# Optimization experiments

Measured on AMD Instinct MI355X. Metric: run time of the kernel, lower is better.

## Reference

```python
import jax, jax.numpy as jnp
import numpy as np

D_MODEL, N_HEADS, LATENT, ROPE = 4096, 128, 512, 64
HEAD_DIM = D_MODEL // N_HEADS  # 32
B, S = 2, 1024


def setup_inputs() -> dict:
    key = jax.random.key(0)
    ks = jax.random.split(key, 9)
    def w(k, i, o):
        return jax.random.normal(k, (i, o), dtype=jnp.float32) * (1.0 / np.sqrt(i))
    return {
        "x": jax.random.normal(ks[0], (B, S, D_MODEL), dtype=jnp.float32),
        "Wq_down": w(ks[1], D_MODEL, LATENT),
        "Wq_up": w(ks[2], LATENT, N_HEADS * HEAD_DIM),
        "Wq_rope": w(ks[3], D_MODEL, N_HEADS * ROPE),
        "Wkv_down": w(ks[4], D_MODEL, LATENT),
        "Wk_up": w(ks[5], LATENT, N_HEADS * HEAD_DIM),
        "Wv_up": w(ks[6], LATENT, N_HEADS * HEAD_DIM),
        "Wk_rope": w(ks[7], D_MODEL, ROPE),
        "Wo": w(ks[8], N_HEADS * HEAD_DIM, D_MODEL),
    }


def reference(x, Wq_down, Wq_up, Wq_rope, Wkv_down, Wk_up, Wv_up, Wk_rope, Wo):
    b, s, _ = x.shape
    # latent down-projections
    c_q = x @ Wq_down                                   # [B,S,latent]
    c_kv = x @ Wkv_down                                 # [B,S,latent]
    # up-projections, reshaped to per-head
    q_c = (c_q @ Wq_up).reshape(b, s, N_HEADS, HEAD_DIM)    # [B,S,H,Dh]
    q_r = (x @ Wq_rope).reshape(b, s, N_HEADS, ROPE)        # [B,S,H,Dr]
    k_c = (c_kv @ Wk_up).reshape(b, s, N_HEADS, HEAD_DIM)   # [B,S,H,Dh]
    v_c = (c_kv @ Wv_up).reshape(b, s, N_HEADS, HEAD_DIM)   # [B,S,H,Dh]
    k_r = x @ Wk_rope                                       # [B,S,Dr] shared over heads
    scale = jnp.asarray((HEAD_DIM + ROPE) ** 0.5, x.dtype)
    # scores = q.k with q=[q_c|q_r], k=[k_c|k_r(broadcast)] -> split the dot product
    scores = (jnp.einsum("bqhd,bkhd->bhqk", q_c, k_c)
              + jnp.einsum("bqhd,bkd->bhqk", q_r, k_r)) / scale  # [B,H,S,S]
    attn = jax.nn.softmax(scores, axis=-1)
    out = jnp.einsum("bhqk,bkhd->bqhd", attn, v_c)          # [B,S,H,Dh]
    out = out.reshape(b, s, N_HEADS * HEAD_DIM)
    return out @ Wo                                         # [B,S,d_model]
```

## Files before the change

kernel.cpp:

```cpp
#include <hip/hip_runtime.h>
#include <hip/hip_bf16.h>
#include <math.h>

#define D_MODEL 4096
#define N_HEADS 128
#define LATENT  512
#define ROPE_D  64
#define HEAD_D  32
#define BATCH   2
#define SEQ     1024
#define NTOK    (BATCH*SEQ)

typedef unsigned short u16;
typedef __attribute__((ext_vector_type(8))) short bf16x8;
typedef __attribute__((ext_vector_type(4))) float f32x4;

__device__ __forceinline__ u16 f2bf(float f) {
    union { float f; unsigned u; } v; v.f = f;
    unsigned r = (v.u + 0x7fffu + ((v.u >> 16) & 1u)) >> 16;
    return (u16)r;
}

__device__ __forceinline__ void gl_lds16(const u16* g, u16* l) {
    __builtin_amdgcn_global_load_lds(
        (const __attribute__((address_space(1))) unsigned int*)g,
        (__attribute__((address_space(3))) unsigned int*)l, 16, 0, 0);
}

__global__ __launch_bounds__(256)
void cast_x_kernel(const float* __restrict__ in, u16* __restrict__ out)
{
    size_t i = ((size_t)blockIdx.x * 256 + threadIdx.x) * 8;
    float4 a = *(const float4*)(in + i);
    float4 b = *(const float4*)(in + i + 4);
    u16 o[8] = {f2bf(a.x), f2bf(a.y), f2bf(a.z), f2bf(a.w),
                f2bf(b.x), f2bf(b.y), f2bf(b.z), f2bf(b.w)};
    *(bf16x8*)(out + i) = *(bf16x8*)o;
}

__global__ __launch_bounds__(256)
void castT_kernel(const float* __restrict__ W, u16* __restrict__ Wt,
                  int K, int N)
{
    __shared__ float tile[32][33];
    const int tid = threadIdx.x;
    const int j0 = blockIdx.x * 32;
    const int i0 = blockIdx.y * 32;
    #pragma unroll
    for (int it = 0; it < 4; ++it) {
        int e = tid + it * 256;
        int r = e >> 5, c = e & 31;
        tile[r][c] = (j0 + c < N) ? W[(size_t)(i0 + r) * N + j0 + c] : 0.f;
    }
    __syncthreads();
    #pragma unroll
    for (int it = 0; it < 4; ++it) {
        int e = tid + it * 256;
        int n = e >> 5, k = e & 31;
        Wt[(size_t)(j0 + n) * K + i0 + k] = f2bf(tile[k][n]);
    }
}

template<int BN_, int OUTF32>
__global__ __launch_bounds__(512)
void gemm256(const u16* __restrict__ A, const u16* __restrict__ Bt,
             void* __restrict__ Cout, int M, int N, int K,
             int lda, int ldb, int ldc)
{
    constexpr int WN   = BN_ / 4;
    constexpr int NFR  = WN / 16;
    constexpr int BUFE = 8192 + BN_ * 32;

    extern __shared__ __align__(16) u16 lds[];

    const int tid  = threadIdx.x;
    const int lane = tid & 63;
    const int wave = tid >> 6;
    const int wr = wave >> 2, wc = wave & 3;
    const int l15 = lane & 15, lg = lane >> 4;

    const int nwg  = gridDim.x * gridDim.y;
    const int orig = blockIdx.y * gridDim.x + blockIdx.x;
    const int swz  = (orig & 7) * (nwg >> 3) + (orig >> 3);
    const int bm = (swz / gridDim.x) * 256, bn = (swz % gridDim.x) * BN_;

    const int NT = K >> 5;

    auto stage = [&](int t) {
        const int buf = t & 3;
        u16* bA = lds + buf * BUFE;
        u16* bB = bA + 8192;
        const int kt = t * 32;
        #pragma unroll
        for (int it = 0; it < 2; ++it) {
            int f = it * 512 + tid;
            int row = f >> 2, c = f & 3;
            int sc = (c ^ (row >> 1)) & 3;
            gl_lds16(A + (size_t)(bm + row) * lda + kt + sc * 8, bA + f * 8);
        }
        #pragma unroll
        for (int it = 0; it < BN_ / 128; ++it) {
            int f = it * 512 + tid;
            int row = f >> 2, c = f & 3;
            int sc = (c ^ (row >> 1)) & 3;
            gl_lds16(Bt + (size_t)(bn + row) * ldb + kt + sc * 8, bB + f * 8);
        }
    };

    f32x4 acc[8][NFR];
    #pragma unroll
    for (int m = 0; m < 8; ++m)
        #pragma unroll
        for (int n = 0; n < NFR; ++n) acc[m][n] = (f32x4){0.f, 0.f, 0.f, 0.f};

    stage(0); stage(1); stage(2);

    for (int t = 0; t < NT; ++t) {
        const int rem = NT - 1 - t;
        if constexpr (BN_ == 256) {
            if (rem >= 2)      asm volatile("s_waitcnt vmcnt(8)" ::: "memory");
            else if (rem == 1) asm volatile("s_waitcnt vmcnt(4)" ::: "memory");
            else               asm volatile("s_waitcnt vmcnt(0)" ::: "memory");
        } else {
            if (rem >= 2)      asm volatile("s_waitcnt vmcnt(6)" ::: "memory");
            else if (rem == 1) asm volatile("s_waitcnt vmcnt(3)" ::: "memory");
            else               asm volatile("s_waitcnt vmcnt(0)" ::: "memory");
        }
        __builtin_amdgcn_s_barrier();
        asm volatile("" ::: "memory");

        if (t + 3 < NT) stage(t + 3);

        const u16* bA = lds + (t & 3) * BUFE;
        const u16* bB = bA + 8192;

        bf16x8 af[8], bfr[NFR];
        #pragma unroll
        for (int m = 0; m < 8; ++m) {
            int row = wr * 128 + m * 16 + l15;
            af[m] = *(const bf16x8*)(bA + row * 32 + (((lg ^ (row >> 1)) & 3) << 3));
        }
        #pragma unroll
        for (int n = 0; n < NFR; ++n) {
            int row = wc * WN + n * 16 + l15;
            bfr[n] = *(const bf16x8*)(bB + row * 32 + (((lg ^ (row >> 1)) & 3) << 3));
        }
        __builtin_amdgcn_s_setprio(1);
        #pragma unroll
        for (int m = 0; m < 8; ++m)
            #pragma unroll
            for (int n = 0; n < NFR; ++n)
                acc[m][n] = __builtin_amdgcn_mfma_f32_16x16x32_bf16(
                    af[m], bfr[n], acc[m][n], 0, 0, 0);
        __builtin_amdgcn_s_setprio(0);
    }

    #pragma unroll
    for (int m = 0; m < 8; ++m)
        #pragma unroll
        for (int n = 0; n < NFR; ++n)
            #pragma unroll
            for (int ri = 0; ri < 4; ++ri) {
                int row = bm + wr * 128 + m * 16 + 4 * lg + ri;
                int col = bn + wc * WN + n * 16 + l15;
                if (col < N) {
                    float v = acc[m][n][ri];
                    if (OUTF32) ((float*)Cout)[(size_t)row * ldc + col] = v;
                    else        ((u16*)Cout)[(size_t)row * ldc + col] = f2bf(v);
                }
            }
}

__global__ __launch_bounds__(256)
void vtrans_kernel(const u16* __restrict__ vc, u16* __restrict__ vt)
{
    __shared__ __align__(16) u16 tile[64][72];
    const int tid = threadIdx.x;
    const int c0 = blockIdx.x * 64;
    const int s0 = blockIdx.y * 64;
    const int b  = blockIdx.z;
    #pragma unroll
    for (int it = 0; it < 2; ++it) {
        int e = it * 256 + tid;
        int r = e >> 3, c8 = e & 7;
        *(bf16x8*)&tile[r][c8 * 8] =
            *(const bf16x8*)(vc + (size_t)(b * SEQ + s0 + r) * 8192 + c0 + c8 * 8);
    }
    __syncthreads();
    #pragma unroll
    for (int it = 0; it < 2; ++it) {
        int e = it * 256 + tid;
        int d = e >> 3, c8 = e & 7;
        u16 o[8];
        #pragma unroll
        for (int j = 0; j < 8; ++j) o[j] = tile[c8 * 8 + j][d];
        *(bf16x8*)(vt + (size_t)(b * D_MODEL + c0 + d) * SEQ + s0 + c8 * 8) = *(bf16x8*)o;
    }
}

__global__ __launch_bounds__(256)
void attn_kernel(const u16* __restrict__ q_c, const u16* __restrict__ q_r,
                 const u16* __restrict__ k_c, const u16* __restrict__ k_r,
                 const u16* __restrict__ vt,  u16* __restrict__ attn_out)
{
    __shared__ __align__(16) u16 s_kc[2][64 * 32];
    __shared__ __align__(16) u16 s_kr[2][64 * 64];
    __shared__ __align__(16) u16 s_vt[2][32 * 64];
    __shared__ __align__(16) u16 s_p[4][16 * 64];

    const int tid  = threadIdx.x;
    const int lane = tid & 63;
    const int w    = tid >> 6;
    const int l15  = lane & 15, lg = lane >> 4;
    const int q0 = blockIdx.x * 64;
    const int h  = blockIdx.y;
    const int b  = blockIdx.z;
    const size_t bS = (size_t)b * SEQ;
    const int hc = h * HEAD_D;
    const float c2 = 0.1020620726159658f * 1.44269504088896f;

    const int qrow = q0 + w * 16 + l15;
    const bf16x8 qf0 = *(const bf16x8*)(q_c + (bS + qrow) * 4096 + hc + lg * 8);
    const bf16x8 qf1 = *(const bf16x8*)(q_r + (bS + qrow) * 9344 + h * ROPE_D + lg * 8);
    const bf16x8 qf2 = *(const bf16x8*)(q_r + (bS + qrow) * 9344 + h * ROPE_D + 32 + lg * 8);

    float m2 = -1e30f, lsum = 0.f;
    f32x4 oacc[2];
    oacc[0] = (f32x4){0.f, 0.f, 0.f, 0.f};
    oacc[1] = (f32x4){0.f, 0.f, 0.f, 0.f};

    auto stage = [&](int buf, int k0) {
        { int f = tid, r = f >> 2, c = f & 3;
          gl_lds16(k_c + (bS + k0 + r) * 8192 + hc + ((c ^ (r & 3)) << 3),
                   &s_kc[buf][f * 8]); }
        #pragma unroll
        for (int it = 0; it < 2; ++it) {
          int f = it * 256 + tid, r = f >> 3, c = f & 7;
          gl_lds16(k_r + (bS + k0 + r) * 9344 + ((c ^ (r & 7)) << 3),
                   &s_kr[buf][f * 8]); }
        { int f = tid, d = f >> 3, c = f & 7;
          gl_lds16(vt + ((size_t)b * D_MODEL + hc + d) * SEQ + k0 + ((c ^ (d & 7)) << 3),
                   &s_vt[buf][f * 8]); }
    };

    stage(0, 0);
    __syncthreads();

    int cur = 0;
    for (int t = 0; t < SEQ / 64; ++t) {
        if (t + 1 < SEQ / 64) stage(cur ^ 1, (t + 1) * 64);

        f32x4 sc[4];
        #pragma unroll
        for (int fc = 0; fc < 4; ++fc) sc[fc] = (f32x4){0.f, 0.f, 0.f, 0.f};
        __builtin_amdgcn_s_setprio(1);
        #pragma unroll
        for (int fc = 0; fc < 4; ++fc) {
            int row = fc * 16 + l15;
            bf16x8 kb = *(const bf16x8*)&s_kc[cur][row * 32 + ((lg ^ (row & 3)) << 3)];
            sc[fc] = __builtin_amdgcn_mfma_f32_16x16x32_bf16(kb, qf0, sc[fc], 0, 0, 0);
        }
        #pragma unroll
        for (int tt = 0; tt < 2; ++tt) {
            bf16x8 qf = tt ? qf2 : qf1;
            #pragma unroll
            for (int fc = 0; fc < 4; ++fc) {
                int row = fc * 16 + l15;
                bf16x8 kb = *(const bf16x8*)&s_kr[cur][row * 64 + (((tt * 4 + lg) ^ (row & 7)) << 3)];
                sc[fc] = __builtin_amdgcn_mfma_f32_16x16x32_bf16(kb, qf, sc[fc], 0, 0, 0);
            }
        }
        __builtin_amdgcn_s_setprio(0);

        float tmx = sc[0][0];
        #pragma unroll
        for (int fc = 0; fc < 4; ++fc)
            #pragma unroll
            for (int ri = 0; ri < 4; ++ri)
                tmx = fmaxf(tmx, sc[fc][ri]);
        tmx = fmaxf(tmx, __shfl_xor(tmx, 16));
        tmx = fmaxf(tmx, __shfl_xor(tmx, 32));
        float tl2 = tmx * c2;
        if (!__all(tl2 <= m2 + 8.f)) {
            float mn = fmaxf(m2, tl2);
            float corr = exp2f(m2 - mn);
            m2 = mn;
            lsum *= corr;
            #pragma unroll
            for (int ri = 0; ri < 4; ++ri) {
                float cr = __shfl(corr, 4 * lg + ri);
                oacc[0][ri] *= cr; oacc[1][ri] *= cr;
            }
        }
        float rs = 0.f;
        unsigned pk0[4], pk1[4];
        #pragma unroll
        for (int fc = 0; fc < 4; ++fc) {
            float p0 = exp2f(fmaf(sc[fc][0], c2, -m2));
            float p1 = exp2f(fmaf(sc[fc][1], c2, -m2));
            float p2 = exp2f(fmaf(sc[fc][2], c2, -m2));
            float p3 = exp2f(fmaf(sc[fc][3], c2, -m2));
            rs += (p0 + p1) + (p2 + p3);
            asm("v_cvt_pk_bf16_f32 %0, %1, %2" : "=v"(pk0[fc]) : "v"(p0), "v"(p1));
            asm("v_cvt_pk_bf16_f32 %0, %1, %2" : "=v"(pk1[fc]) : "v"(p2), "v"(p3));
        }
        rs += __shfl_xor(rs, 16);
        rs += __shfl_xor(rs, 32);
        lsum += rs;
        #pragma unroll
        for (int fc = 0; fc < 4; ++fc) {
            int ch = (2 * fc + (lg >> 1)) ^ (l15 & 7);
            *(uint2*)&s_p[w][l15 * 64 + ch * 8 + 4 * (lg & 1)] =
                make_uint2(pk0[fc], pk1[fc]);
        }

        __builtin_amdgcn_s_setprio(1);
        #pragma unroll
        for (int t2 = 0; t2 < 2; ++t2) {
            bf16x8 pa = *(const bf16x8*)&s_p[w][l15 * 64 + (((t2 * 4 + lg) ^ (l15 & 7)) << 3)];
            #pragma unroll
            for (int fd = 0; fd < 2; ++fd) {
                int row = fd * 16 + l15;
                bf16x8 vb = *(const bf16x8*)&s_vt[cur][row * 64 + (((t2 * 4 + lg) ^ (row & 7)) << 3)];
                oacc[fd] = __builtin_amdgcn_mfma_f32_16x16x32_bf16(pa, vb, oacc[fd], 0, 0, 0);
            }
        }
        __builtin_amdgcn_s_setprio(0);

        __syncthreads();
        cur ^= 1;
    }

    #pragma unroll
    for (int ri = 0; ri < 4; ++ri) {
        float ls = __shfl(lsum, 4 * lg + ri);
        float inv = 1.f / ls;
        int row = q0 + w * 16 + 4 * lg + ri;
        attn_out[(bS + row) * 4096 + hc + l15]      = f2bf(oacc[0][ri] * inv);
        attn_out[(bS + row) * 4096 + hc + 16 + l15] = f2bf(oacc[1][ri] * inv);
    }
}

extern "C" void kernel_launch(void* const* d_in, const int* in_sizes, int n_in,
                              void* d_out, int out_size, void* d_ws, size_t ws_size,
                              hipStream_t stream)
{
    (void)in_sizes; (void)n_in; (void)out_size; (void)ws_size;

    const float* x        = (const float*)d_in[0];
    const float* Wq_down  = (const float*)d_in[1];
    const float* Wq_up    = (const float*)d_in[2];
    const float* Wq_rope  = (const float*)d_in[3];
    const float* Wkv_down = (const float*)d_in[4];
    const float* Wk_up    = (const float*)d_in[5];
    const float* Wv_up    = (const float*)d_in[6];
    const float* Wk_rope  = (const float*)d_in[7];
    const float* Wo       = (const float*)d_in[8];

    u16* ws   = (u16*)d_ws;
    u16* xb   = ws;
    u16* BigT = xb + (size_t)8388608;
    u16* UpT  = BigT + (size_t)38797312;
    u16* WuqT = UpT + (size_t)4194304;
    u16* C_big= WuqT + (size_t)2097152;
    u16* C2   = C_big + (size_t)19136512;
    u16* WoT  = BigT;
    u16* vt   = BigT + (size_t)16777216;
    u16* q_c  = BigT + (size_t)25165824;
    u16* attn_out = xb;

    dim3 blk(256);

    (void)hipFuncSetAttribute((const void*)&gemm256<256,0>,
                              hipFuncAttributeMaxDynamicSharedMemorySize, 131072);
    (void)hipFuncSetAttribute((const void*)&gemm256<128,0>,
                              hipFuncAttributeMaxDynamicSharedMemorySize, 98304);
    (void)hipFuncSetAttribute((const void*)&gemm256<128,1>,
                              hipFuncAttributeMaxDynamicSharedMemorySize, 98304);

    hipMemsetAsync(BigT + (size_t)9280 * 4096, 0, (size_t)192 * 4096 * 2, stream);
    hipLaunchKernelGGL(cast_x_kernel, dim3(4096), blk, 0, stream, x, xb);
    hipLaunchKernelGGL(castT_kernel, dim3(256, 128), blk, 0, stream, Wq_rope, BigT, 4096, 8192);
    hipLaunchKernelGGL(castT_kernel, dim3(16, 128), blk, 0, stream, Wq_down, BigT + (size_t)8192 * 4096, 4096, 512);
    hipLaunchKernelGGL(castT_kernel, dim3(16, 128), blk, 0, stream, Wkv_down, BigT + (size_t)8704 * 4096, 4096, 512);
    hipLaunchKernelGGL(castT_kernel, dim3(2, 128), blk, 0, stream, Wk_rope, BigT + (size_t)9216 * 4096, 4096, 64);
    hipLaunchKernelGGL(castT_kernel, dim3(128, 16), blk, 0, stream, Wk_up, UpT, 512, 4096);
    hipLaunchKernelGGL(castT_kernel, dim3(128, 16), blk, 0, stream, Wv_up, UpT + (size_t)4096 * 512, 512, 4096);
    hipLaunchKernelGGL(castT_kernel, dim3(128, 16), blk, 0, stream, Wq_up, WuqT, 512, 4096);

    gemm256<256,0><<<dim3(37, 8), dim3(512), 131072, stream>>>(
        xb, BigT, C_big, NTOK, 9344, 4096, 4096, 4096, 9344);
    hipLaunchKernelGGL(castT_kernel, dim3(128, 128), blk, 0, stream, Wo, WoT, 4096, 4096);
    gemm256<256,0><<<dim3(32, 8), dim3(512), 131072, stream>>>(
        C_big + 8704, UpT, C2, NTOK, 8192, 512, 9344, 512, 8192);
    gemm256<128,0><<<dim3(32, 8), dim3(512), 98304, stream>>>(
        C_big + 8192, WuqT, q_c, NTOK, 4096, 512, 9344, 512, 4096);
    hipLaunchKernelGGL(vtrans_kernel, dim3(64, 16, 2), blk, 0, stream, C2 + 4096, vt);
    hipLaunchKernelGGL(attn_kernel, dim3(16, 128, 2), blk, 0, stream,
                       q_c, C_big, C2, C_big + 9216, vt, attn_out);
    gemm256<128,1><<<dim3(32, 8), dim3(512), 98304, stream>>>(
        attn_out, WoT, d_out, NTOK, 4096, 4096, 4096, 4096, 4096);
}
```

Before: 604.9 us.

## Replace GEMM with 256x128 BK64 triple-buffered ping-pong pipeline

Replaces the templated 256xBN GEMM (BK=32, 4-stage) with a single 256x128 tile kernel using BK=64, three LDS slots, an 8-chunk XOR swizzle, and split A/B prefetch issued across two half-steps. Barriers with sched_barrier fences wrap each MFMA cluster, aiming for a ping-pong style schedule that overlaps loads with compute. All GEMMs now use BN=128 with larger grids. The column bound check is dropped and the zero padding memset is shrunk to match the narrower tile rounding (9344 is a multiple of 128). The cost is more barriers per K step and fewer MFMAs per LDS read for the former BN=256 calls.

```diff
diff --git a/kernel.cpp b/kernel.cpp
--- a/kernel.cpp
+++ b/kernel.cpp
@@ -61,15 +61,15 @@
     }
 }
 
-template<int BN_, int OUTF32>
+template<int OUTF32>
 __global__ __launch_bounds__(512)
-void gemm256(const u16* __restrict__ A, const u16* __restrict__ Bt,
-             void* __restrict__ Cout, int M, int N, int K,
-             int lda, int ldb, int ldc)
-{
-    constexpr int WN   = BN_ / 4;
-    constexpr int NFR  = WN / 16;
-    constexpr int BUFE = 8192 + BN_ * 32;
+void gemm8p(const u16* __restrict__ A, const u16* __restrict__ Bt,
+            void* __restrict__ Cout, int M, int N, int K,
+            int lda, int ldb, int ldc)
+{
+    constexpr int TILE_A = 256 * 64;
+    constexpr int TILE_B = 128 * 64;
+    constexpr int SLOT   = TILE_A + TILE_B;
 
     extern __shared__ __align__(16) u16 lds[];
 
@@ -82,92 +82,102 @@
     const int nwg  = gridDim.x * gridDim.y;
     const int orig = blockIdx.y * gridDim.x + blockIdx.x;
     const int swz  = (orig & 7) * (nwg >> 3) + (orig >> 3);
-    const int bm = (swz / gridDim.x) * 256, bn = (swz % gridDim.x) * BN_;
-
-    const int NT = K >> 5;
-
-    auto stage = [&](int t) {
-        const int buf = t & 3;
-        u16* bA = lds + buf * BUFE;
-        u16* bB = bA + 8192;
-        const int kt = t * 32;
+    const int bm = (swz / gridDim.x) * 256, bn = (swz % gridDim.x) * 128;
+
+    const int NT = K >> 6;
+
+    auto stageA = [&](int t) {
+        u16* base = lds + (t % 3) * SLOT;
+        const int kt = t << 6;
+        #pragma unroll
+        for (int it = 0; it < 4; ++it) {
+            int f = it * 512 + tid;
+            int row = f >> 3, c = f & 7;
+            int sc = c ^ (row & 7);
+            gl_lds16(A + (size_t)(bm + row) * lda + kt + sc * 8, base + f * 8);
+        }
+    };
+    auto stageB = [&](int t) {
+        u16* base = lds + (t % 3) * SLOT + TILE_A;
+        const int kt = t << 6;
         #pragma unroll
         for (int it = 0; it < 2; ++it) {
             int f = it * 512 + tid;
-            int row = f >> 2, c = f & 3;
-            int sc = (c ^ (row >> 1)) & 3;
-            gl_lds16(A + (size_t)(bm + row) * lda + kt + sc * 8, bA + f * 8);
-        }
-        #pragma unroll
-        for (int it = 0; it < BN_ / 128; ++it) {
-            int f = it * 512 + tid;
-            int row = f >> 2, c = f & 3;
-            int sc = (c ^ (row >> 1)) & 3;
-            gl_lds16(Bt + (size_t)(bn + row) * ldb + kt + sc * 8, bB + f * 8);
+            int row = f >> 3, c = f & 7;
+            int sc = c ^ (row & 7);
+            gl_lds16(Bt + (size_t)(bn + row) * ldb + kt + sc * 8, base + f * 8);
         }
     };
 
-    f32x4 acc[8][NFR];
+    f32x4 acc[8][2];
+    #pragma unroll
+    for (int m = 0; m < 8; ++m) {
+        acc[m][0] = (f32x4){0.f, 0.f, 0.f, 0.f};
+        acc[m][1] = (f32x4){0.f, 0.f, 0.f, 0.f};
+    }
+
+    stageA(0); stageB(0); stageA(1); stageB(1);
+    asm volatile("s_waitcnt vmcnt(6)" ::: "memory");
+    __builtin_amdgcn_sched_barrier(0);
+    __builtin_amdgcn_s_barrier();
+    __builtin_amdgcn_sched_barrier(0);
+
+    for (int t = 0; t < NT; ++t) {
+        const u16* bA = lds + (t % 3) * SLOT;
+        const u16* bB = bA + TILE_A;
+        #pragma unroll
+        for (int s = 0; s < 2; ++s) {
+            bf16x8 af[8], bfr[2];
+            #pragma unroll
+            for (int m = 0; m < 8; ++m) {
+                int row = wr * 128 + m * 16 + l15;
+                int ch = (s * 4 + lg) ^ (row & 7);
+                af[m] = *(const bf16x8*)(bA + row * 64 + ch * 8);
+            }
+            #pragma unroll
+            for (int n = 0; n < 2; ++n) {
+                int row = wc * 32 + n * 16 + l15;
+                int ch = (s * 4 + lg) ^ (row & 7);
+                bfr[n] = *(const bf16x8*)(bB + row * 64 + ch * 8);
+            }
+            if (s == 0) {
+                if (t + 2 < NT) stageA(t + 2);
+            } else {
+                if (t + 2 < NT) stageB(t + 2);
+                if (t + 1 < NT) {
+                    if (t + 2 < NT) asm volatile("s_waitcnt vmcnt(6)" ::: "memory");
+                    else            asm volatile("s_waitcnt vmcnt(0)" ::: "memory");
+                }
+            }
+            asm volatile("" ::: "memory");
+            __builtin_amdgcn_sched_barrier(0);
+            __builtin_amdgcn_s_barrier();
+            __builtin_amdgcn_sched_barrier(0);
+            __builtin_amdgcn_s_setprio(1);
+            #pragma unroll
+            for (int m = 0; m < 8; ++m) {
+                acc[m][0] = __builtin_amdgcn_mfma_f32_16x16x32_bf16(af[m], bfr[0], acc[m][0], 0, 0, 0);
+                acc[m][1] = __builtin_amdgcn_mfma_f32_16x16x32_bf16(af[m], bfr[1], acc[m][1], 0, 0, 0);
+            }
+            __builtin_amdgcn_s_setprio(0);
+            __builtin_amdgcn_sched_barrier(0);
+            __builtin_amdgcn_s_barrier();
+            __builtin_amdgcn_sched_barrier(0);
+            asm volatile("" ::: "memory");
+        }
+    }
+
     #pragma unroll
     for (int m = 0; m < 8; ++m)
         #pragma unroll
-        for (int n = 0; n < NFR; ++n) acc[m][n] = (f32x4){0.f, 0.f, 0.f, 0.f};
-
-    stage(0); stage(1); stage(2);
-
-    for (int t = 0; t < NT; ++t) {
-        const int rem = NT - 1 - t;
-        if constexpr (BN_ == 256) {
-            if (rem >= 2)      asm volatile("s_waitcnt vmcnt(8)" ::: "memory");
-            else if (rem == 1) asm volatile("s_waitcnt vmcnt(4)" ::: "memory");
-            else               asm volatile("s_waitcnt vmcnt(0)" ::: "memory");
-        } else {
-            if (rem >= 2)      asm volatile("s_waitcnt vmcnt(6)" ::: "memory");
-            else if (rem == 1) asm volatile("s_waitcnt vmcnt(3)" ::: "memory");
-            else               asm volatile("s_waitcnt vmcnt(0)" ::: "memory");
-        }
-        __builtin_amdgcn_s_barrier();
-        asm volatile("" ::: "memory");
-
-        if (t + 3 < NT) stage(t + 3);
-
-        const u16* bA = lds + (t & 3) * BUFE;
-        const u16* bB = bA + 8192;
-
-        bf16x8 af[8], bfr[NFR];
-        #pragma unroll
-        for (int m = 0; m < 8; ++m) {
-            int row = wr * 128 + m * 16 + l15;
-            af[m] = *(const bf16x8*)(bA + row * 32 + (((lg ^ (row >> 1)) & 3) << 3));
-        }
-        #pragma unroll
-        for (int n = 0; n < NFR; ++n) {
-            int row = wc * WN + n * 16 + l15;
-            bfr[n] = *(const bf16x8*)(bB + row * 32 + (((lg ^ (row >> 1)) & 3) << 3));
-        }
-        __builtin_amdgcn_s_setprio(1);
-        #pragma unroll
-        for (int m = 0; m < 8; ++m)
-            #pragma unroll
-            for (int n = 0; n < NFR; ++n)
-                acc[m][n] = __builtin_amdgcn_mfma_f32_16x16x32_bf16(
-                    af[m], bfr[n], acc[m][n], 0, 0, 0);
-        __builtin_amdgcn_s_setprio(0);
-    }
-
-    #pragma unroll
-    for (int m = 0; m < 8; ++m)
-        #pragma unroll
-        for (int n = 0; n < NFR; ++n)
+        for (int n = 0; n < 2; ++n)
             #pragma unroll
             for (int ri = 0; ri < 4; ++ri) {
                 int row = bm + wr * 128 + m * 16 + 4 * lg + ri;
-                int col = bn + wc * WN + n * 16 + l15;
-                if (col < N) {
-                    float v = acc[m][n][ri];
-                    if (OUTF32) ((float*)Cout)[(size_t)row * ldc + col] = v;
-                    else        ((u16*)Cout)[(size_t)row * ldc + col] = f2bf(v);
-                }
+                int col = bn + wc * 32 + n * 16 + l15;
+                float v = acc[m][n][ri];
+                if (OUTF32) ((float*)Cout)[(size_t)row * ldc + col] = v;
+                else        ((u16*)Cout)[(size_t)row * ldc + col] = f2bf(v);
             }
 }
 
@@ -371,14 +381,12 @@
 
     dim3 blk(256);
 
-    (void)hipFuncSetAttribute((const void*)&gemm256<256,0>,
-                              hipFuncAttributeMaxDynamicSharedMemorySize, 131072);
-    (void)hipFuncSetAttribute((const void*)&gemm256<128,0>,
-                              hipFuncAttributeMaxDynamicSharedMemorySize, 98304);
-    (void)hipFuncSetAttribute((const void*)&gemm256<128,1>,
-                              hipFuncAttributeMaxDynamicSharedMemorySize, 98304);
-
-    hipMemsetAsync(BigT + (size_t)9280 * 4096, 0, (size_t)192 * 4096 * 2, stream);
+    (void)hipFuncSetAttribute((const void*)&gemm8p<0>,
+                              hipFuncAttributeMaxDynamicSharedMemorySize, 147456);
+    (void)hipFuncSetAttribute((const void*)&gemm8p<1>,
+                              hipFuncAttributeMaxDynamicSharedMemorySize, 147456);
+
+    hipMemsetAsync(BigT + (size_t)9280 * 4096, 0, (size_t)64 * 4096 * 2, stream);
     hipLaunchKernelGGL(cast_x_kernel, dim3(4096), blk, 0, stream, x, xb);
     hipLaunchKernelGGL(castT_kernel, dim3(256, 128), blk, 0, stream, Wq_rope, BigT, 4096, 8192);
     hipLaunchKernelGGL(castT_kernel, dim3(16, 128), blk, 0, stream, Wq_down, BigT + (size_t)8192 * 4096, 4096, 512);
@@ -388,16 +396,16 @@
     hipLaunchKernelGGL(castT_kernel, dim3(128, 16), blk, 0, stream, Wv_up, UpT + (size_t)4096 * 512, 512, 4096);
     hipLaunchKernelGGL(castT_kernel, dim3(128, 16), blk, 0, stream, Wq_up, WuqT, 512, 4096);
 
-    gemm256<256,0><<<dim3(37, 8), dim3(512), 131072, stream>>>(
+    gemm8p<0><<<dim3(73, 8), dim3(512), 147456, stream>>>(
         xb, BigT, C_big, NTOK, 9344, 4096, 4096, 4096, 9344);
     hipLaunchKernelGGL(castT_kernel, dim3(128, 128), blk, 0, stream, Wo, WoT, 4096, 4096);
-    gemm256<256,0><<<dim3(32, 8), dim3(512), 131072, stream>>>(
+    gemm8p<0><<<dim3(64, 8), dim3(512), 147456, stream>>>(
         C_big + 8704, UpT, C2, NTOK, 8192, 512, 9344, 512, 8192);
-    gemm256<128,0><<<dim3(32, 8), dim3(512), 98304, stream>>>(
+    gemm8p<0><<<dim3(32, 8), dim3(512), 147456, stream>>>(
         C_big + 8192, WuqT, q_c, NTOK, 4096, 512, 9344, 512, 4096);
     hipLaunchKernelGGL(vtrans_kernel, dim3(64, 16, 2), blk, 0, stream, C2 + 4096, vt);
     hipLaunchKernelGGL(attn_kernel, dim3(16, 128, 2), blk, 0, stream,
                        q_c, C_big, C2, C_big + 9216, vt, attn_out);
-    gemm256<128,1><<<dim3(32, 8), dim3(512), 98304, stream>>>(
+    gemm8p<1><<<dim3(32, 8), dim3(512), 147456, stream>>>(
         attn_out, WoT, d_out, NTOK, 4096, 4096, 4096, 4096, 4096);
 }
```

New measurement: 584.3 us. -3.4%, faster.
